# Kernel tuning notes

Hardware: AMD Instinct MI355X
Metric: run time of the kernel (lower is better)

The kernel has to match this reference:

```python
import jax, jax.numpy as jnp
import numpy as np

EPS = 1e-12  # tf.nn.l2_normalize epsilon

def _l2_normalize(x, axis):
    sq = jnp.sum(jnp.square(x), axis=axis, keepdims=True)
    return x * jax.lax.rsqrt(jnp.maximum(sq, EPS))

def setup_inputs() -> dict:
    key = jax.random.key(0)
    k1, k2 = jax.random.split(key)
    B, C, CLS = 8192, 512, 32000
    inputs = jax.random.normal(k1, (B, C), dtype=jnp.float32)
    # glorot_uniform for shape (C, CLS)
    limit = np.sqrt(6.0 / (C + CLS)).astype(np.float32)
    w = jax.random.uniform(k2, (C, CLS), dtype=jnp.float32, minval=-limit, maxval=limit)
    return {"inputs": inputs, "w": w}

def reference(inputs, w):
    # x: [B, C] l2-normalized over channel; w: [C, CLS] l2-normalized over channel.
    # The original broadcast-multiply-reduce over the channel axis == matmul.
    x = _l2_normalize(inputs, axis=-1)
    wn = _l2_normalize(w, axis=0)
    return jnp.einsum('bc,ck->bk', x, wn)  # [B, CLS] cosine similarities
```

## Files before the change

### kernel.cpp

```cpp
#include <hip/hip_runtime.h>
#include <hip/hip_bf16.h>
#include <stdint.h>

#define M_DIM 8192
#define K_DIM 512
#define N_DIM 32000

typedef short bf16x8 __attribute__((ext_vector_type(8)));
typedef float f32x4 __attribute__((ext_vector_type(4)));
typedef unsigned short u16;

__device__ __forceinline__ u16 f2bf(float f) {
  union { float f; uint32_t u; } v; v.f = f;
  uint32_t r = (v.u + 0x7fffu + ((v.u >> 16) & 1u)) >> 16;
  return (u16)r;
}

__global__ void k_zero(float* __restrict__ cn) {
  cn[blockIdx.x * 256 + threadIdx.x] = 0.f;
}

__global__ void k_xnorm(const float* __restrict__ x, u16* __restrict__ xn) {
  int row = (blockIdx.x * blockDim.x + threadIdx.x) >> 6;
  int lane = threadIdx.x & 63;
  const float4* rp = (const float4*)(x + (size_t)row * K_DIM);
  float4 a = rp[lane];
  float4 b = rp[lane + 64];
  float s = a.x*a.x + a.y*a.y + a.z*a.z + a.w*a.w
          + b.x*b.x + b.y*b.y + b.z*b.z + b.w*b.w;
#pragma unroll
  for (int off = 32; off > 0; off >>= 1) s += __shfl_xor(s, off, 64);
  float r = rsqrtf(fmaxf(s, 1e-12f));
  ushort4 o0 = make_ushort4(f2bf(a.x*r), f2bf(a.y*r), f2bf(a.z*r), f2bf(a.w*r));
  ushort4 o1 = make_ushort4(f2bf(b.x*r), f2bf(b.y*r), f2bf(b.z*r), f2bf(b.w*r));
  ushort4* dst = (ushort4*)(xn + (size_t)row * K_DIM);
  dst[lane] = o0;
  dst[lane + 64] = o1;
}

__global__ void k_wtrans(const float* __restrict__ w, float* __restrict__ cn,
                         u16* __restrict__ wT) {
  __shared__ u16 tile[64][68];
  int c0 = blockIdx.x * 64;
  int r0 = blockIdx.y * 64;
  int tc = threadIdx.x & 63;
  int tw = threadIdx.x >> 6;
  float s = 0.f;
#pragma unroll
  for (int i = 0; i < 16; ++i) {
    int r = i * 4 + tw;
    float v = w[(size_t)(r0 + r) * N_DIM + c0 + tc];
    s = fmaf(v, v, s);
    tile[tc][r] = f2bf(v);
  }
  atomicAdd(&cn[c0 + tc], s);
  __syncthreads();
  int cc = threadIdx.x >> 4;
  int rr = (threadIdx.x & 15) * 4;
#pragma unroll
  for (int i = 0; i < 4; ++i) {
    int c = cc + i * 16;
    ushort4 v = *(const ushort4*)&tile[c][rr];
    *(ushort4*)(wT + (size_t)(c0 + c) * K_DIM + r0 + rr) = v;
  }
}

__global__ __launch_bounds__(512, 2) void k_gemm(const u16* __restrict__ A,
                                                 const u16* __restrict__ Bt,
                                                 const float* __restrict__ cn,
                                                 float* __restrict__ C) {
  __shared__ u16 sm[2][32768];
  constexpr int BOFF = 16384;

  const int b = blockIdx.x;
  const int xcd = b & 7;
  const int cu = b >> 3;
  const int bm = xcd * 4 + (cu & 3);
  const int bn0 = cu >> 2;
  const int cnt = (bn0 < 5) ? 16 : 15;

  const int tid = threadIdx.x;
  const int lane = tid & 63;
  const int w = tid >> 6;
  const int wr = w >> 2;
  const int wc = w & 3;
  const int la = lane & 15;
  const int lk = lane >> 4;
  const int rx = la & 7;
  const int s0 = ((0 + lk) ^ rx) * 8;
  const int s1 = ((4 + lk) ^ rx) * 8;

  const int srow = tid >> 3;
  const int sgl = ((tid & 7) ^ (srow & 7)) * 8;
  const int ldst = srow * 64 + (tid & 7) * 8;
  const int arow0 = (wr * 128 + la) * 64;
  const int brow0 = (wc * 64 + la) * 64;

  const u16* ag = A + (size_t)(bm * 256 + srow) * K_DIM + sgl;
  int bn = bn0;
  const u16* bg = Bt + (size_t)(bn * 256 + srow) * K_DIM + sgl;
  constexpr size_t BSTEP = (size_t)8 * 256 * K_DIM;

  f32x4 acc[8][4] = {};

#pragma unroll
  for (int i = 0; i < 4; ++i)
    __builtin_amdgcn_global_load_lds(
        (const __attribute__((address_space(1))) void*)(ag + (size_t)i * 64 * K_DIM),
        (__attribute__((address_space(3))) void*)&sm[0][i * 4096 + ldst], 16, 0, 0);
#pragma unroll
  for (int i = 0; i < 4; ++i)
    __builtin_amdgcn_global_load_lds(
        (const __attribute__((address_space(1))) void*)(bg + (size_t)i * 64 * K_DIM),
        (__attribute__((address_space(3))) void*)&sm[0][BOFF + i * 4096 + ldst], 16, 0, 0);
  __syncthreads();

  for (int ti = 0; ti < cnt; ++ti) {
    const bool last_tile = (ti + 1 == cnt);

    for (int kt = 0; kt < 8; ++kt) {
      const int cur = kt & 1;
      const int nxt = cur ^ 1;
      const bool pf = (kt < 7) || !last_tile;
      const u16* agk = (kt < 7) ? (ag + (kt + 1) * 64) : ag;
      const u16* bgk = (kt < 7) ? (bg + (kt + 1) * 64) : (bg + BSTEP);

      bf16x8 bf[4][2];

      {
#pragma unroll
        for (int n = 0; n < 4; ++n) {
          bf[n][0] = *(const bf16x8*)&sm[cur][BOFF + brow0 + n * 1024 + s0];
          bf[n][1] = *(const bf16x8*)&sm[cur][BOFF + brow0 + n * 1024 + s1];
        }
        bf16x8 af[2][2];
#pragma unroll
        for (int m = 0; m < 2; ++m) {
          af[m][0] = *(const bf16x8*)&sm[cur][arow0 + m * 1024 + s0];
          af[m][1] = *(const bf16x8*)&sm[cur][arow0 + m * 1024 + s1];
        }
        if (pf) {
#pragma unroll
          for (int i = 0; i < 4; ++i)
            __builtin_amdgcn_global_load_lds(
                (const __attribute__((address_space(1))) void*)(agk + (size_t)i * 64 * K_DIM),
                (__attribute__((address_space(3))) void*)&sm[nxt][i * 4096 + ldst], 16, 0, 0);
        }
        __builtin_amdgcn_s_barrier();
        asm volatile("s_waitcnt lgkmcnt(0)" ::: "memory");
        __builtin_amdgcn_sched_barrier(0);
        __builtin_amdgcn_s_setprio(1);
#pragma unroll
        for (int m = 0; m < 2; ++m)
#pragma unroll
          for (int n = 0; n < 4; ++n) {
            acc[m][n] = __builtin_amdgcn_mfma_f32_16x16x32_bf16(af[m][0], bf[n][0], acc[m][n], 0, 0, 0);
            acc[m][n] = __builtin_amdgcn_mfma_f32_16x16x32_bf16(af[m][1], bf[n][1], acc[m][n], 0, 0, 0);
          }
        __builtin_amdgcn_s_setprio(0);
        __builtin_amdgcn_s_barrier();
      }

#pragma unroll
      for (int p = 1; p < 4; ++p) {
        bf16x8 af[2][2];
#pragma unroll
        for (int m = 0; m < 2; ++m) {
          af[m][0] = *(const bf16x8*)&sm[cur][arow0 + (p * 2 + m) * 1024 + s0];
          af[m][1] = *(const bf16x8*)&sm[cur][arow0 + (p * 2 + m) * 1024 + s1];
        }
        if (p == 1 && pf) {
#pragma unroll
          for (int i = 0; i < 4; ++i)
            __builtin_amdgcn_global_load_lds(
                (const __attribute__((address_space(1))) void*)(bgk + (size_t)i * 64 * K_DIM),
                (__attribute__((address_space(3))) void*)&sm[nxt][BOFF + i * 4096 + ldst], 16, 0, 0);
        }
        __builtin_amdgcn_s_barrier();
        asm volatile("s_waitcnt lgkmcnt(0)" ::: "memory");
        __builtin_amdgcn_sched_barrier(0);
        __builtin_amdgcn_s_setprio(1);
#pragma unroll
        for (int m = 0; m < 2; ++m)
#pragma unroll
          for (int n = 0; n < 4; ++n) {
            acc[p * 2 + m][n] = __builtin_amdgcn_mfma_f32_16x16x32_bf16(af[m][0], bf[n][0], acc[p * 2 + m][n], 0, 0, 0);
            acc[p * 2 + m][n] = __builtin_amdgcn_mfma_f32_16x16x32_bf16(af[m][1], bf[n][1], acc[p * 2 + m][n], 0, 0, 0);
          }
        __builtin_amdgcn_s_setprio(0);
        if (p < 3) __builtin_amdgcn_s_barrier();
      }

      __syncthreads();
    }

    {
      const size_t crow0 = (size_t)bm * 256 + wr * 128 + lk * 4;
      const int ccol0 = bn * 256 + wc * 64 + la;
      float rs[4];
#pragma unroll
      for (int n = 0; n < 4; ++n)
        rs[n] = rsqrtf(fmaxf(cn[ccol0 + n * 16], 1e-12f));
#pragma unroll
      for (int m = 0; m < 8; ++m)
#pragma unroll
        for (int j = 0; j < 4; ++j) {
          float* cp = C + (crow0 + m * 16 + j) * N_DIM + ccol0;
#pragma unroll
          for (int n = 0; n < 4; ++n)
            __builtin_nontemporal_store(acc[m][n][j] * rs[n], cp + n * 16);
        }
#pragma unroll
      for (int m = 0; m < 8; ++m)
#pragma unroll
        for (int n = 0; n < 4; ++n)
          acc[m][n] = (f32x4){0.f, 0.f, 0.f, 0.f};
    }

    bn += 8;
    bg += BSTEP;
  }
}

extern "C" void kernel_launch(void* const* d_in, const int* in_sizes, int n_in,
                              void* d_out, int out_size, void* d_ws, size_t ws_size,
                              hipStream_t stream) {
  const float* x = (const float*)d_in[0];
  const float* w = (const float*)d_in[1];
  float* out = (float*)d_out;

  char* ws = (char*)d_ws;
  float* cn = (float*)ws;
  u16* xn = (u16*)(ws + 131072);
  u16* wT = (u16*)(ws + 131072 + (size_t)M_DIM * K_DIM * 2);

  k_zero<<<N_DIM / 256, 256, 0, stream>>>(cn);
  k_xnorm<<<M_DIM / 4, 256, 0, stream>>>(x, xn);
  k_wtrans<<<dim3(N_DIM / 64, K_DIM / 64), 256, 0, stream>>>(w, cn, wT);
  k_gemm<<<256, 512, 0, stream>>>(xn, wT, cn, out);
}
```

Baseline: 375.2 us.

## Shrink GEMM block tile to 128x128 with 256 threads and simplified pipeline

Changes the GEMM from 256x256 tiles with 8 waves to 128x128 tiles with 4 waves, doubling the grid to 512 blocks and remapping blocks to row/column tiles. The inner k-step is simplified: both A and B prefetches for the next stage are issued up front, and the sub-phase barriers and priority hints are removed. The intent is lower per-block register and LDS pressure and less synchronisation overhead. The cost is less data reuse per loaded byte, so more LDS and L2 traffic per MFMA.

```diff
diff --git a/kernel.cpp b/kernel.cpp
--- a/kernel.cpp
+++ b/kernel.cpp
@@ -65,25 +65,25 @@
   }
 }
 
-__global__ __launch_bounds__(512, 2) void k_gemm(const u16* __restrict__ A,
+__global__ __launch_bounds__(256, 2) void k_gemm(const u16* __restrict__ A,
                                                  const u16* __restrict__ Bt,
                                                  const float* __restrict__ cn,
                                                  float* __restrict__ C) {
-  __shared__ u16 sm[2][32768];
-  constexpr int BOFF = 16384;
+  __shared__ u16 sm[2][16384];
+  constexpr int BOFF = 8192;
 
   const int b = blockIdx.x;
   const int xcd = b & 7;
-  const int cu = b >> 3;
-  const int bm = xcd * 4 + (cu & 3);
-  const int bn0 = cu >> 2;
-  const int cnt = (bn0 < 5) ? 16 : 15;
+  const int blk = b >> 3;
+  const int bm = xcd * 8 + (blk & 7);
+  const int bn0 = blk >> 3;
+  const int cnt = (bn0 < 2) ? 32 : 31;
 
   const int tid = threadIdx.x;
   const int lane = tid & 63;
   const int w = tid >> 6;
-  const int wr = w >> 2;
-  const int wc = w & 3;
+  const int wr = w >> 1;
+  const int wc = w & 1;
   const int la = lane & 15;
   const int lk = lane >> 4;
   const int rx = la & 7;
@@ -93,26 +93,25 @@
   const int srow = tid >> 3;
   const int sgl = ((tid & 7) ^ (srow & 7)) * 8;
   const int ldst = srow * 64 + (tid & 7) * 8;
-  const int arow0 = (wr * 128 + la) * 64;
+  const int arow0 = (wr * 64 + la) * 64;
   const int brow0 = (wc * 64 + la) * 64;
 
-  const u16* ag = A + (size_t)(bm * 256 + srow) * K_DIM + sgl;
+  const u16* ag = A + (size_t)(bm * 128 + srow) * K_DIM + sgl;
   int bn = bn0;
-  const u16* bg = Bt + (size_t)(bn * 256 + srow) * K_DIM + sgl;
-  constexpr size_t BSTEP = (size_t)8 * 256 * K_DIM;
-
-  f32x4 acc[8][4] = {};
-
-#pragma unroll
-  for (int i = 0; i < 4; ++i)
-    __builtin_amdgcn_global_load_lds(
-        (const __attribute__((address_space(1))) void*)(ag + (size_t)i * 64 * K_DIM),
-        (__attribute__((address_space(3))) void*)&sm[0][i * 4096 + ldst], 16, 0, 0);
-#pragma unroll
-  for (int i = 0; i < 4; ++i)
-    __builtin_amdgcn_global_load_lds(
-        (const __attribute__((address_space(1))) void*)(bg + (size_t)i * 64 * K_DIM),
-        (__attribute__((address_space(3))) void*)&sm[0][BOFF + i * 4096 + ldst], 16, 0, 0);
+  const u16* bg = Bt + (size_t)(bn * 128 + srow) * K_DIM + sgl;
+  constexpr size_t BSTEP = (size_t)8 * 128 * K_DIM;
+
+  f32x4 acc[4][4] = {};
+
+#define GLL(p, eoff)                                                              \
+  __builtin_amdgcn_global_load_lds(                                              \
+      (const __attribute__((address_space(1))) void*)(p),                        \
+      (__attribute__((address_space(3))) void*)&sm[0][(eoff)], 16, 0, 0)
+
+#pragma unroll
+  for (int i = 0; i < 4; ++i) GLL(ag + (size_t)i * 32 * K_DIM, i * 2048 + ldst);
+#pragma unroll
+  for (int i = 0; i < 4; ++i) GLL(bg + (size_t)i * 32 * K_DIM, BOFF + i * 2048 + ldst);
   __syncthreads();
 
   for (int ti = 0; ti < cnt; ++ti) {
@@ -125,84 +124,46 @@
       const u16* agk = (kt < 7) ? (ag + (kt + 1) * 64) : ag;
       const u16* bgk = (kt < 7) ? (bg + (kt + 1) * 64) : (bg + BSTEP);
 
-      bf16x8 bf[4][2];
-
-      {
+      if (pf) {
+        const int nb = nxt * 16384;
+#pragma unroll
+        for (int i = 0; i < 4; ++i) GLL(agk + (size_t)i * 32 * K_DIM, nb + i * 2048 + ldst);
+#pragma unroll
+        for (int i = 0; i < 4; ++i) GLL(bgk + (size_t)i * 32 * K_DIM, nb + BOFF + i * 2048 + ldst);
+      }
+
+      bf16x8 af[4][2], bf[4][2];
+#pragma unroll
+      for (int m = 0; m < 4; ++m) {
+        af[m][0] = *(const bf16x8*)&sm[cur][arow0 + m * 1024 + s0];
+        af[m][1] = *(const bf16x8*)&sm[cur][arow0 + m * 1024 + s1];
+      }
+#pragma unroll
+      for (int n = 0; n < 4; ++n) {
+        bf[n][0] = *(const bf16x8*)&sm[cur][BOFF + brow0 + n * 1024 + s0];
+        bf[n][1] = *(const bf16x8*)&sm[cur][BOFF + brow0 + n * 1024 + s1];
+      }
+
+#pragma unroll
+      for (int m = 0; m < 4; ++m)
 #pragma unroll
         for (int n = 0; n < 4; ++n) {
-          bf[n][0] = *(const bf16x8*)&sm[cur][BOFF + brow0 + n * 1024 + s0];
-          bf[n][1] = *(const bf16x8*)&sm[cur][BOFF + brow0 + n * 1024 + s1];
+          acc[m][n] = __builtin_amdgcn_mfma_f32_16x16x32_bf16(af[m][0], bf[n][0], acc[m][n], 0, 0, 0);
+          acc[m][n] = __builtin_amdgcn_mfma_f32_16x16x32_bf16(af[m][1], bf[n][1], acc[m][n], 0, 0, 0);
         }
-        bf16x8 af[2][2];
-#pragma unroll
-        for (int m = 0; m < 2; ++m) {
-          af[m][0] = *(const bf16x8*)&sm[cur][arow0 + m * 1024 + s0];
-          af[m][1] = *(const bf16x8*)&sm[cur][arow0 + m * 1024 + s1];
-        }
-        if (pf) {
-#pragma unroll
-          for (int i = 0; i < 4; ++i)
-            __builtin_amdgcn_global_load_lds(
-                (const __attribute__((address_space(1))) void*)(agk + (size_t)i * 64 * K_DIM),
-                (__attribute__((address_space(3))) void*)&sm[nxt][i * 4096 + ldst], 16, 0, 0);
-        }
-        __builtin_amdgcn_s_barrier();
-        asm volatile("s_waitcnt lgkmcnt(0)" ::: "memory");
-        __builtin_amdgcn_sched_barrier(0);
-        __builtin_amdgcn_s_setprio(1);
-#pragma unroll
-        for (int m = 0; m < 2; ++m)
-#pragma unroll
-          for (int n = 0; n < 4; ++n) {
-            acc[m][n] = __builtin_amdgcn_mfma_f32_16x16x32_bf16(af[m][0], bf[n][0], acc[m][n], 0, 0, 0);
-            acc[m][n] = __builtin_amdgcn_mfma_f32_16x16x32_bf16(af[m][1], bf[n][1], acc[m][n], 0, 0, 0);
-          }
-        __builtin_amdgcn_s_setprio(0);
-        __builtin_amdgcn_s_barrier();
-      }
-
-#pragma unroll
-      for (int p = 1; p < 4; ++p) {
-        bf16x8 af[2][2];
-#pragma unroll
-        for (int m = 0; m < 2; ++m) {
-          af[m][0] = *(const bf16x8*)&sm[cur][arow0 + (p * 2 + m) * 1024 + s0];
-          af[m][1] = *(const bf16x8*)&sm[cur][arow0 + (p * 2 + m) * 1024 + s1];
-        }
-        if (p == 1 && pf) {
-#pragma unroll
-          for (int i = 0; i < 4; ++i)
-            __builtin_amdgcn_global_load_lds(
-                (const __attribute__((address_space(1))) void*)(bgk + (size_t)i * 64 * K_DIM),
-                (__attribute__((address_space(3))) void*)&sm[nxt][BOFF + i * 4096 + ldst], 16, 0, 0);
-        }
-        __builtin_amdgcn_s_barrier();
-        asm volatile("s_waitcnt lgkmcnt(0)" ::: "memory");
-        __builtin_amdgcn_sched_barrier(0);
-        __builtin_amdgcn_s_setprio(1);
-#pragma unroll
-        for (int m = 0; m < 2; ++m)
-#pragma unroll
-          for (int n = 0; n < 4; ++n) {
-            acc[p * 2 + m][n] = __builtin_amdgcn_mfma_f32_16x16x32_bf16(af[m][0], bf[n][0], acc[p * 2 + m][n], 0, 0, 0);
-            acc[p * 2 + m][n] = __builtin_amdgcn_mfma_f32_16x16x32_bf16(af[m][1], bf[n][1], acc[p * 2 + m][n], 0, 0, 0);
-          }
-        __builtin_amdgcn_s_setprio(0);
-        if (p < 3) __builtin_amdgcn_s_barrier();
-      }
 
       __syncthreads();
     }
 
     {
-      const size_t crow0 = (size_t)bm * 256 + wr * 128 + lk * 4;
-      const int ccol0 = bn * 256 + wc * 64 + la;
+      const size_t crow0 = (size_t)bm * 128 + wr * 64 + lk * 4;
+      const int ccol0 = bn * 128 + wc * 64 + la;
       float rs[4];
 #pragma unroll
       for (int n = 0; n < 4; ++n)
         rs[n] = rsqrtf(fmaxf(cn[ccol0 + n * 16], 1e-12f));
 #pragma unroll
-      for (int m = 0; m < 8; ++m)
+      for (int m = 0; m < 4; ++m)
 #pragma unroll
         for (int j = 0; j < 4; ++j) {
           float* cp = C + (crow0 + m * 16 + j) * N_DIM + ccol0;
@@ -211,7 +172,7 @@
             __builtin_nontemporal_store(acc[m][n][j] * rs[n], cp + n * 16);
         }
 #pragma unroll
-      for (int m = 0; m < 8; ++m)
+      for (int m = 0; m < 4; ++m)
 #pragma unroll
         for (int n = 0; n < 4; ++n)
           acc[m][n] = (f32x4){0.f, 0.f, 0.f, 0.f};
@@ -220,6 +181,7 @@
     bn += 8;
     bg += BSTEP;
   }
+#undef GLL
 }
 
 extern "C" void kernel_launch(void* const* d_in, const int* in_sizes, int n_in,
@@ -237,5 +199,5 @@
   k_zero<<<N_DIM / 256, 256, 0, stream>>>(cn);
   k_xnorm<<<M_DIM / 4, 256, 0, stream>>>(x, xn);
   k_wtrans<<<dim3(N_DIM / 64, K_DIM / 64), 256, 0, stream>>>(w, cn, wT);
-  k_gemm<<<256, 512, 0, stream>>>(xn, wT, cn, out);
-}
+  k_gemm<<<512, 256, 0, stream>>>(xn, wT, cn, out);
+}
```

Result: faster. 355.8 us (-5.1%).
